# Optimization experiments

Hardware: AMD Instinct MI355X
Metric: run time of the kernel (lower is better)

## Reference

```python
import jax, jax.numpy as jnp
import numpy as np

T, D, N, W = 8192, 768, 10000, 32  # tokens, hidden dim, num spans, max span width


def setup_inputs() -> dict:
    key = jax.random.key(0)
    k1, k2, k3, k4, k5 = jax.random.split(key, 5)
    sentence_embeddings = jax.random.normal(k1, (T, D), dtype=jnp.float32)
    lengths = jax.random.randint(k2, (N,), 1, W + 1)           # span lengths in [1, W]
    starts = jax.random.randint(k3, (N,), 0, T - W)
    ends = starts + lengths - 1                                 # inclusive end, < T
    sentence_spans = jnp.stack([starts, ends], axis=1).astype(jnp.int32)
    Wq = (jax.random.normal(k4, (D, D), dtype=jnp.float32) / np.sqrt(D).astype(np.float32))
    bq = jax.random.normal(k5, (D,), dtype=jnp.float32) * 0.01
    return {"sentence_embeddings": sentence_embeddings,
            "sentence_spans": sentence_spans,
            "Wq": Wq, "bq": bq}


def reference(sentence_embeddings, sentence_spans, Wq, bq):
    # Padded + masked batched version of the per-span loop:
    #   span_emb = emb[s:e+1]; q = span_emb @ Wq.T + bq
    #   w = softmax(q @ span_emb.T, dim=1); out = (w @ span_emb).sum(0)
    starts = sentence_spans[:, 0]                               # [N]
    lengths = sentence_spans[:, 1] - starts + 1                 # inclusive end -> length
    offs = jnp.arange(W)
    pos = starts[:, None] + offs[None, :]                       # [N, W] token indices
    valid = offs[None, :] < lengths[:, None]                    # [N, W] in-span mask
    pos = jnp.clip(pos, 0, sentence_embeddings.shape[0] - 1)
    span_emb = sentence_embeddings[pos]                         # [N, W, D] ragged gather
    span_emb = jnp.where(valid[:, :, None], span_emb, 0.0)
    query = jnp.einsum('nwd,ed->nwe', span_emb, Wq) + bq        # [N, W, D]
    scores = jnp.einsum('nqd,nkd->nqk', query, span_emb)        # [N, W, W]
    scores = jnp.where(valid[:, None, :], scores, -jnp.inf)     # mask pad keys (softmax dim=1)
    weights = jax.nn.softmax(scores, axis=-1)
    attn = jnp.einsum('nqk,nkd->nqd', weights, span_emb)        # [N, W, D]
    attn = jnp.where(valid[:, :, None], attn, 0.0)              # drop pad query rows
    return attn.sum(axis=1)                                     # [N, D] == torch.sum(attention, dim=0) per span
```

## Files before the change

### kernel.cpp

```cpp
#include <hip/hip_runtime.h>
#include <hip/hip_bf16.h>
#include <cstddef>
#include <cstdint>

constexpr int Tt = 8192;
constexpr int Dd = 768;
constexpr int Nn = 10000;
constexpr int Ww = 32;

typedef __bf16 bf16x8 __attribute__((ext_vector_type(8)));
typedef __bf16 bf16x4 __attribute__((ext_vector_type(4)));
typedef __bf16 bf16x2 __attribute__((ext_vector_type(2)));
typedef _Float16 half8v __attribute__((ext_vector_type(8)));
typedef _Float16 half4v __attribute__((ext_vector_type(4)));
typedef float f32x4 __attribute__((ext_vector_type(4)));

#define MFMA16(a, b, c) __builtin_amdgcn_mfma_f32_16x16x32_bf16((a), (b), (c), 0, 0, 0)
#define MFMAH(a, b, c) __builtin_amdgcn_mfma_f32_16x16x32_f16((a), (b), (c), 0, 0, 0)

template <bool LO>
__global__ __launch_bounds__(256) void conv_kernel(const float* __restrict__ src,
                                                   __bf16* __restrict__ h,
                                                   __bf16* __restrict__ l, int n4) {
    const int i = blockIdx.x * 256 + threadIdx.x;
    if (i >= n4) return;
    const float4 v = reinterpret_cast<const float4*>(src)[i];
    bf16x4 oh, ol;
    oh[0] = (__bf16)v.x; oh[1] = (__bf16)v.y; oh[2] = (__bf16)v.z; oh[3] = (__bf16)v.w;
    reinterpret_cast<bf16x4*>(h)[i] = oh;
    if (LO) {
        ol[0] = (__bf16)(v.x - (float)oh[0]);
        ol[1] = (__bf16)(v.y - (float)oh[1]);
        ol[2] = (__bf16)(v.z - (float)oh[2]);
        ol[3] = (__bf16)(v.w - (float)oh[3]);
        reinterpret_cast<bf16x4*>(l)[i] = ol;
    }
}

__global__ __launch_bounds__(256) void conv3_kernel(const float* __restrict__ src,
                                                    __bf16* __restrict__ h,
                                                    __bf16* __restrict__ l,
                                                    _Float16* __restrict__ f, int n4) {
    const int i = blockIdx.x * 256 + threadIdx.x;
    if (i >= n4) return;
    const float4 v = reinterpret_cast<const float4*>(src)[i];
    bf16x4 oh, ol;
    half4v of;
    const float vv[4] = {v.x, v.y, v.z, v.w};
#pragma unroll
    for (int j = 0; j < 4; ++j) {
        oh[j] = (__bf16)vv[j];
        ol[j] = (__bf16)(vv[j] - (float)oh[j]);
        of[j] = (_Float16)vv[j];
    }
    reinterpret_cast<bf16x4*>(h)[i] = oh;
    reinterpret_cast<bf16x4*>(l)[i] = ol;
    reinterpret_cast<half4v*>(f)[i] = of;
}

__global__ __launch_bounds__(256) void zero_kernel(int* __restrict__ p, int n) {
    const int i = blockIdx.x * 256 + threadIdx.x;
    if (i < n) p[i] = 0;
}

__global__ __launch_bounds__(256) void hist_kernel(const int* __restrict__ spans,
                                                   int* __restrict__ hist) {
    const int i = blockIdx.x * 256 + threadIdx.x;
    if (i < Nn) atomicAdd(&hist[spans[2 * i]], 1);
}

__global__ __launch_bounds__(256) void scan_kernel(int* __restrict__ hist) {
    __shared__ int part[256];
    const int t = threadIdx.x;
    int vals[32];
    int sum = 0;
#pragma unroll
    for (int i = 0; i < 32; ++i) { vals[i] = hist[t * 32 + i]; sum += vals[i]; }
    part[t] = sum;
    __syncthreads();
    for (int off = 1; off < 256; off <<= 1) {
        const int v = (t >= off) ? part[t - off] : 0;
        __syncthreads();
        part[t] += v;
        __syncthreads();
    }
    int run = (t == 0) ? 0 : part[t - 1];
#pragma unroll
    for (int i = 0; i < 32; ++i) { const int v = vals[i]; hist[t * 32 + i] = run; run += v; }
}

__global__ __launch_bounds__(256) void scatter_kernel(const int* __restrict__ spans,
                                                      int* __restrict__ offs,
                                                      int* __restrict__ perm) {
    const int i = blockIdx.x * 256 + threadIdx.x;
    if (i < Nn) {
        const int p = atomicAdd(&offs[spans[2 * i]], 1);
        perm[p] = i;
    }
}

template <bool SPLIT>
__global__ __launch_bounds__(256) void qproj_kernel(const float* __restrict__ emb,
                                                    const float* __restrict__ Wq,
                                                    const float* __restrict__ bq,
                                                    __bf16* __restrict__ Qh,
                                                    __bf16* __restrict__ Ql) {
    __shared__ float As[64][32];
    __shared__ float Bs[64][32];
    const int tid = threadIdx.x;
    const int tx = tid & 15;
    const int ty = tid >> 4;
    const int m0 = blockIdx.x * 64;
    const int n0 = blockIdx.y * 64;

    float acc[4][4] = {};

    for (int kc = 0; kc < Dd; kc += 32) {
#pragma unroll
        for (int i = 0; i < 2; ++i) {
            const int f   = tid + i * 256;
            const int row = f >> 3;
            const int c4  = f & 7;
            const int ph  = (c4 + (row >> 2)) & 7;
            *reinterpret_cast<float4*>(&As[row][ph * 4]) =
                *reinterpret_cast<const float4*>(&emb[(size_t)(m0 + row) * Dd + kc + c4 * 4]);
            *reinterpret_cast<float4*>(&Bs[row][ph * 4]) =
                *reinterpret_cast<const float4*>(&Wq[(size_t)(n0 + row) * Dd + kc + c4 * 4]);
        }
        __syncthreads();
#pragma unroll
        for (int d4 = 0; d4 < 8; ++d4) {
            float4 av[4], bv[4];
#pragma unroll
            for (int r = 0; r < 4; ++r)
                av[r] = *reinterpret_cast<const float4*>(&As[ty * 4 + r][((d4 + ty) & 7) * 4]);
#pragma unroll
            for (int c = 0; c < 4; ++c)
                bv[c] = *reinterpret_cast<const float4*>(&Bs[tx * 4 + c][((d4 + tx) & 7) * 4]);
#pragma unroll
            for (int r = 0; r < 4; ++r)
#pragma unroll
                for (int c = 0; c < 4; ++c) {
                    acc[r][c] += av[r].x * bv[c].x;
                    acc[r][c] += av[r].y * bv[c].y;
                    acc[r][c] += av[r].z * bv[c].z;
                    acc[r][c] += av[r].w * bv[c].w;
                }
        }
        __syncthreads();
    }
#pragma unroll
    for (int r = 0; r < 4; ++r) {
        bf16x4 oh, ol;
#pragma unroll
        for (int c = 0; c < 4; ++c) {
            const float v = acc[r][c] + bq[n0 + tx * 4 + c];
            const __bf16 h = (__bf16)v;
            oh[c] = h;
            if (SPLIT) ol[c] = (__bf16)(v - (float)h);
        }
        const size_t off = (size_t)(m0 + ty * 4 + r) * Dd + n0 + tx * 4;
        *reinterpret_cast<bf16x4*>(&Qh[off]) = oh;
        if (SPLIT) *reinterpret_cast<bf16x4*>(&Ql[off]) = ol;
    }
}

__global__ __launch_bounds__(256) void qproj_mfma2_kernel(const __bf16* __restrict__ Eh,
                                                          const __bf16* __restrict__ El,
                                                          const __bf16* __restrict__ Wh,
                                                          const __bf16* __restrict__ Wl,
                                                          const float* __restrict__ bq,
                                                          _Float16* __restrict__ Qf) {
    __shared__ __align__(16) __bf16 Ahs[128 * 32];
    __shared__ __align__(16) __bf16 Als[128 * 32];
    __shared__ __align__(16) __bf16 Bhs[64 * 32];
    __shared__ __align__(16) __bf16 Bls[64 * 32];

    const int tid  = threadIdx.x;
    const int wave = tid >> 6;
    const int lane = tid & 63;

    const int b   = blockIdx.x;
    const int xcd = b & 7;
    const int li  = b >> 3;
    const int mt  = xcd * 8 + li / 12;
    const int nt  = li % 12;
    const int m0 = mt * 128;
    const int n0 = nt * 64;
    const int wm = (wave & 1) * 64;
    const int wn = (wave >> 1) * 32;
    const int fr = lane & 15;
    const int kg = lane >> 4;

    int arow[2], agc[2];
#pragma unroll
    for (int i = 0; i < 2; ++i) {
        const int seg = tid + i * 256;
        arow[i] = seg >> 2;
        agc[i]  = ((seg & 3) ^ (arow[i] & 3)) * 8;
    }
    const int brow = tid >> 2;
    const int bgc  = ((tid & 3) ^ (brow & 3)) * 8;

    bf16x8 pah[2], pal[2], pbh, pbl;
    auto ldnext = [&](int kc) {
#pragma unroll
        for (int i = 0; i < 2; ++i) {
            const size_t ga = (size_t)(m0 + arow[i]) * Dd + kc + agc[i];
            pah[i] = *reinterpret_cast<const bf16x8*>(&Eh[ga]);
            pal[i] = *reinterpret_cast<const bf16x8*>(&El[ga]);
        }
        const size_t gb = (size_t)(n0 + brow) * Dd + kc + bgc;
        pbh = *reinterpret_cast<const bf16x8*>(&Wh[gb]);
        pbl = *reinterpret_cast<const bf16x8*>(&Wl[gb]);
    };
    ldnext(0);

    f32x4 acc[4][2] = {};

    for (int kc = 0; kc < Dd; kc += 32) {
        __syncthreads();
#pragma unroll
        for (int i = 0; i < 2; ++i) {
            const int slot = tid + i * 256;
            *reinterpret_cast<bf16x8*>(&Ahs[slot * 8]) = pah[i];
            *reinterpret_cast<bf16x8*>(&Als[slot * 8]) = pal[i];
        }
        *reinterpret_cast<bf16x8*>(&Bhs[tid * 8]) = pbh;
        *reinterpret_cast<bf16x8*>(&Bls[tid * 8]) = pbl;
        __syncthreads();
        if (kc + 32 < Dd) ldnext(kc + 32);

        bf16x8 ah[4], al[4], bh[2], bl[2];
#pragma unroll
        for (int r = 0; r < 4; ++r) {
            const int R = wm + r * 16 + fr;
            const int p = (kg ^ (R & 3)) * 8;
            ah[r] = *reinterpret_cast<const bf16x8*>(&Ahs[R * 32 + p]);
            al[r] = *reinterpret_cast<const bf16x8*>(&Als[R * 32 + p]);
        }
#pragma unroll
        for (int c = 0; c < 2; ++c) {
            const int R = wn + c * 16 + fr;
            const int p = (kg ^ (R & 3)) * 8;
            bh[c] = *reinterpret_cast<const bf16x8*>(&Bhs[R * 32 + p]);
            bl[c] = *reinterpret_cast<const bf16x8*>(&Bls[R * 32 + p]);
        }
#pragma unroll
        for (int r = 0; r < 4; ++r)
#pragma unroll
            for (int c = 0; c < 2; ++c) {
                acc[r][c] = MFMA16(ah[r], bh[c], acc[r][c]);
                acc[r][c] = MFMA16(al[r], bh[c], acc[r][c]);
                acc[r][c] = MFMA16(ah[r], bl[c], acc[r][c]);
            }
    }

#pragma unroll
    for (int c = 0; c < 2; ++c) {
        const int ocol = n0 + wn + c * 16 + fr;
        const float bqv = bq[ocol];
#pragma unroll
        for (int r = 0; r < 4; ++r)
#pragma unroll
            for (int j = 0; j < 4; ++j) {
                const int orow = m0 + wm + r * 16 + kg * 4 + j;
                Qf[(size_t)orow * Dd + ocol] = (_Float16)(acc[r][c][j] + bqv);
            }
    }
}

__global__ __launch_bounds__(256) void span_attn_win_kernel(const _Float16* __restrict__ Ef,
                                                            const int* __restrict__ spans,
                                                            const _Float16* __restrict__ Qf,
                                                            const int* __restrict__ perm,
                                                            float* __restrict__ out) {
    constexpr int WR = 48, CH = 128, ST = 136, NCH = Dd / CH;
    __shared__ __align__(16) _Float16 Qs[WR * ST];
    __shared__ __align__(16) _Float16 Es[WR * ST];

    const int tid  = threadIdx.x;
    const int wave = tid >> 6;
    const int lane = tid & 63;

    const int b     = blockIdx.x;
    const int bp    = (b & 7) * 313 + (b >> 3);
    const int slot0 = bp * 4;
    const int slot  = slot0 + wave;
    const bool active = slot < Nn;

    int s0 = perm[slot0 < Nn ? slot0 : (Nn - 1)];
    if ((unsigned)s0 >= (unsigned)Nn) s0 = 0;
    int s = active ? perm[slot] : s0;
    if ((unsigned)s >= (unsigned)Nn) s = 0;

    const int w0    = spans[2 * s0];
    const int start = spans[2 * s];
    const int L     = spans[2 * s + 1] - start + 1;
    const bool big  = L > 16;
    const int sl    = start - w0;
    const bool inwin = active && sl >= 0 && sl <= (WR - 32);

    const int row = lane & 15;
    const int kq  = lane >> 4;

    const size_t gq = (size_t)(start + row) * Dd + kq * 8;

    f32x4 acc00 = {0.f, 0.f, 0.f, 0.f};
    f32x4 acc01 = {0.f, 0.f, 0.f, 0.f};
    f32x4 acc10 = {0.f, 0.f, 0.f, 0.f};
    f32x4 acc11 = {0.f, 0.f, 0.f, 0.f};

    for (int c = 0; c < NCH; ++c) {
        const int c0 = c * CH;
        __syncthreads();
#pragma unroll
        for (int i = 0; i < 3; ++i) {
            const int seg = tid + i * 256;
            const int r  = seg >> 4;
            const int cs = seg & 15;
            const int gr = w0 + r < Tt ? w0 + r : Tt - 1;
            const size_t ga = (size_t)gr * Dd + c0 + cs * 8;
            *reinterpret_cast<half8v*>(&Qs[r * ST + cs * 8]) =
                *reinterpret_cast<const half8v*>(&Qf[ga]);
            *reinterpret_cast<half8v*>(&Es[r * ST + cs * 8]) =
                *reinterpret_cast<const half8v*>(&Ef[ga]);
        }
        __syncthreads();

        if (inwin) {
            const int ab = (sl + row) * ST + kq * 8;
#pragma unroll
            for (int j = 0; j < 4; ++j) {
                const int o = j * 32;
                const half8v a0 = *reinterpret_cast<const half8v*>(&Qs[ab + o]);
                const half8v b0 = *reinterpret_cast<const half8v*>(&Es[ab + o]);
                acc00 = MFMAH(a0, b0, acc00);
                if (big) {
                    const half8v a1 = *reinterpret_cast<const half8v*>(&Qs[ab + 16 * ST + o]);
                    const half8v b1 = *reinterpret_cast<const half8v*>(&Es[ab + 16 * ST + o]);
                    acc01 = MFMAH(a0, b1, acc01);
                    acc10 = MFMAH(a1, b0, acc10);
                    acc11 = MFMAH(a1, b1, acc11);
                }
            }
        } else if (active) {
#pragma unroll
            for (int j = 0; j < 4; ++j) {
                const int o = c0 + j * 32;
                const half8v a0 = *reinterpret_cast<const half8v*>(&Qf[gq + o]);
                const half8v b0 = *reinterpret_cast<const half8v*>(&Ef[gq + o]);
                acc00 = MFMAH(a0, b0, acc00);
                if (big) {
                    const half8v a1 = *reinterpret_cast<const half8v*>(&Qf[gq + 16 * Dd + o]);
                    const half8v b1 = *reinterpret_cast<const half8v*>(&Ef[gq + 16 * Dd + o]);
                    acc01 = MFMAH(a0, b1, acc01);
                    acc10 = MFMAH(a1, b0, acc10);
                    acc11 = MFMAH(a1, b1, acc11);
                }
            }
        }
    }

    const float NEG = -1e30f;
    const bool kv0 = row < L;
    const bool kv1 = (16 + row) < L;
    float cA, cB;
    {
        float w00[4], w01[4], w10[4], w11[4];
#pragma unroll
        for (int r = 0; r < 4; ++r) {
            float m = kv0 ? acc00[r] : NEG;
            if (big) m = fmaxf(m, kv1 ? acc01[r] : NEG);
#pragma unroll
            for (int st = 1; st <= 8; st <<= 1) m = fmaxf(m, __shfl_xor(m, st));
            const float e0 = kv0 ? __expf(acc00[r] - m) : 0.f;
            const float e1 = (big && kv1) ? __expf(acc01[r] - m) : 0.f;
            float sum = e0 + e1;
#pragma unroll
            for (int st = 1; st <= 8; st <<= 1) sum += __shfl_xor(sum, st);
            const float inv = 1.f / sum;
            const bool qv = (kq * 4 + r) < L;
            w00[r] = qv ? e0 * inv : 0.f;
            w01[r] = qv ? e1 * inv : 0.f;
            if (big) {
                float mh = kv0 ? acc10[r] : NEG;
                mh = fmaxf(mh, kv1 ? acc11[r] : NEG);
#pragma unroll
                for (int st = 1; st <= 8; st <<= 1) mh = fmaxf(mh, __shfl_xor(mh, st));
                const float f0 = kv0 ? __expf(acc10[r] - mh) : 0.f;
                const float f1 = kv1 ? __expf(acc11[r] - mh) : 0.f;
                float sh = f0 + f1;
#pragma unroll
                for (int st = 1; st <= 8; st <<= 1) sh += __shfl_xor(sh, st);
                const float invh = 1.f / sh;
                const bool qvh = (16 + kq * 4 + r) < L;
                w10[r] = qvh ? f0 * invh : 0.f;
                w11[r] = qvh ? f1 * invh : 0.f;
            }
        }
        float pa = w00[0] + w00[1] + w00[2] + w00[3];
        float pb = 0.f;
        if (big) {
            pa += w10[0] + w10[1] + w10[2] + w10[3];
            pb = w01[0] + w01[1] + w01[2] + w01[3] +
                 w11[0] + w11[1] + w11[2] + w11[3];
        }
        pa += __shfl_xor(pa, 16);
        pa += __shfl_xor(pa, 32);
        if (big) {
            pb += __shfl_xor(pb, 16);
            pb += __shfl_xor(pb, 32);
        }
        cA = pa;
        cB = pb;
    }

    if (active) {
        f32x4 o[3] = {};
        const int KP = (L + 3) & ~3;
        const _Float16* ebase = Ef + (size_t)start * Dd + lane * 4;
        for (int k = 0; k < KP; k += 4) {
            float cv[4];
            half4v ev[4][3];
#pragma unroll
            for (int j = 0; j < 4; ++j) {
                const int kk = k + j;
                cv[j] = (kk < 16) ? __shfl(cA, kk) : __shfl(cB, kk - 16);
#pragma unroll
                for (int i = 0; i < 3; ++i)
                    ev[j][i] = *reinterpret_cast<const half4v*>(ebase + (size_t)kk * Dd + i * 256);
            }
#pragma unroll
            for (int j = 0; j < 4; ++j)
#pragma unroll
                for (int i = 0; i < 3; ++i) {
                    o[i][0] += cv[j] * (float)ev[j][i][0];
                    o[i][1] += cv[j] * (float)ev[j][i][1];
                    o[i][2] += cv[j] * (float)ev[j][i][2];
                    o[i][3] += cv[j] * (float)ev[j][i][3];
                }
        }
#pragma unroll
        for (int i = 0; i < 3; ++i)
            *reinterpret_cast<f32x4*>(&out[(size_t)s * Dd + i * 256 + lane * 4]) = o[i];
    }
}

template <bool SPLIT, bool SORTED>
__global__ __launch_bounds__(256) void span_attn_g_kernel(const __bf16* __restrict__ Eb,
                                                          const int* __restrict__ spans,
                                                          const __bf16* __restrict__ Qh,
                                                          const __bf16* __restrict__ Ql,
                                                          const int* __restrict__ perm,
                                                          float* __restrict__ out) {
    const int wave = threadIdx.x >> 6;
    const int lane = threadIdx.x & 63;

    int s;
    bool active;
    if (SORTED) {
        const int b    = blockIdx.x;
        const int bp   = (b & 7) * 313 + (b >> 3);
        const int slot = bp * 4 + wave;
        active = slot < Nn;
        int sv = active ? perm[slot] : 0;
        if ((unsigned)sv >= (unsigned)Nn) sv = 0;
        s = sv;
    } else {
        s = blockIdx.x * 4 + wave;
        active = true;
    }

    const int start = spans[2 * s];
    const int L     = spans[2 * s + 1] - start + 1;
    const bool big  = L > 16;

    const int row = lane & 15;
    const int kq  = lane >> 4;

    const size_t rbase = (size_t)(start + row) * Dd + kq * 8;
    const __bf16* qh0 = Qh + rbase;
    const __bf16* eb0 = Eb + rbase;
    const __bf16* ql0 = SPLIT ? (Ql + rbase) : nullptr;

    f32x4 acc00 = {0.f, 0.f, 0.f, 0.f};
    f32x4 acc01 = {0.f, 0.f, 0.f, 0.f};
    f32x4 acc10 = {0.f, 0.f, 0.f, 0.f};
    f32x4 acc11 = {0.f, 0.f, 0.f, 0.f};

    if (!big) {
        for (int kc = 0; kc < Dd; kc += 128) {
            bf16x8 A[4], B[4], AL[4];
#pragma unroll
            for (int j = 0; j < 4; ++j) {
                const int o = kc + j * 32;
                A[j] = *reinterpret_cast<const bf16x8*>(qh0 + o);
                B[j] = *reinterpret_cast<const bf16x8*>(eb0 + o);
                if (SPLIT) AL[j] = *reinterpret_cast<const bf16x8*>(ql0 + o);
            }
#pragma unroll
            for (int j = 0; j < 4; ++j) {
                acc00 = MFMA16(A[j], B[j], acc00);
                if (SPLIT) acc00 = MFMA16(AL[j], B[j], acc00);
            }
        }
    } else {
        for (int kc = 0; kc < Dd; kc += 64) {
            bf16x8 A0[2], A1[2], B0[2], B1[2], AL0[2], AL1[2];
#pragma unroll
            for (int j = 0; j < 2; ++j) {
                const int o = kc + j * 32;
                A0[j] = *reinterpret_cast<const bf16x8*>(qh0 + o);
                A1[j] = *reinterpret_cast<const bf16x8*>(qh0 + 16 * Dd + o);
                B0[j] = *reinterpret_cast<const bf16x8*>(eb0 + o);
                B1[j] = *reinterpret_cast<const bf16x8*>(eb0 + 16 * Dd + o);
                if (SPLIT) {
                    AL0[j] = *reinterpret_cast<const bf16x8*>(ql0 + o);
                    AL1[j] = *reinterpret_cast<const bf16x8*>(ql0 + 16 * Dd + o);
                }
            }
#pragma unroll
            for (int j = 0; j < 2; ++j) {
                acc00 = MFMA16(A0[j], B0[j], acc00);
                acc01 = MFMA16(A0[j], B1[j], acc01);
                acc10 = MFMA16(A1[j], B0[j], acc10);
                acc11 = MFMA16(A1[j], B1[j], acc11);
                if (SPLIT) {
                    acc00 = MFMA16(AL0[j], B0[j], acc00);
                    acc01 = MFMA16(AL0[j], B1[j], acc01);
                    acc10 = MFMA16(AL1[j], B0[j], acc10);
                    acc11 = MFMA16(AL1[j], B1[j], acc11);
                }
            }
        }
    }

    const float NEG = -1e30f;
    const bool kv0 = row < L;
    const bool kv1 = (16 + row) < L;
    float cA, cB;
    {
        float w00[4], w01[4], w10[4], w11[4];
#pragma unroll
        for (int r = 0; r < 4; ++r) {
            float m = kv0 ? acc00[r] : NEG;
            if (big) m = fmaxf(m, kv1 ? acc01[r] : NEG);
#pragma unroll
            for (int st = 1; st <= 8; st <<= 1) m = fmaxf(m, __shfl_xor(m, st));
            const float e0 = kv0 ? __expf(acc00[r] - m) : 0.f;
            const float e1 = (big && kv1) ? __expf(acc01[r] - m) : 0.f;
            float sum = e0 + e1;
#pragma unroll
            for (int st = 1; st <= 8; st <<= 1) sum += __shfl_xor(sum, st);
            const float inv = 1.f / sum;
            const bool qv = (kq * 4 + r) < L;
            w00[r] = qv ? e0 * inv : 0.f;
            w01[r] = qv ? e1 * inv : 0.f;
            if (big) {
                float mh = kv0 ? acc10[r] : NEG;
                mh = fmaxf(mh, kv1 ? acc11[r] : NEG);
#pragma unroll
                for (int st = 1; st <= 8; st <<= 1) mh = fmaxf(mh, __shfl_xor(mh, st));
                const float f0 = kv0 ? __expf(acc10[r] - mh) : 0.f;
                const float f1 = kv1 ? __expf(acc11[r] - mh) : 0.f;
                float sh = f0 + f1;
#pragma unroll
                for (int st = 1; st <= 8; st <<= 1) sh += __shfl_xor(sh, st);
                const float invh = 1.f / sh;
                const bool qvh = (16 + kq * 4 + r) < L;
                w10[r] = qvh ? f0 * invh : 0.f;
                w11[r] = qvh ? f1 * invh : 0.f;
            }
        }
        float pa = w00[0] + w00[1] + w00[2] + w00[3];
        float pb = 0.f;
        if (big) {
            pa += w10[0] + w10[1] + w10[2] + w10[3];
            pb = w01[0] + w01[1] + w01[2] + w01[3] +
                 w11[0] + w11[1] + w11[2] + w11[3];
        }
        pa += __shfl_xor(pa, 16);
        pa += __shfl_xor(pa, 32);
        if (big) {
            pb += __shfl_xor(pb, 16);
            pb += __shfl_xor(pb, 32);
        }
        cA = pa;
        cB = pb;
    }

    if (active) {
        f32x4 o[3] = {};
        const int KP = (L + 3) & ~3;
        const __bf16* ebase = Eb + (size_t)start * Dd + lane * 4;
        for (int k = 0; k < KP; k += 4) {
            float cv[4];
            bf16x4 ev[4][3];
#pragma unroll
            for (int j = 0; j < 4; ++j) {
                const int kk = k + j;
                cv[j] = (kk < 16) ? __shfl(cA, kk) : __shfl(cB, kk - 16);
#pragma unroll
                for (int i = 0; i < 3; ++i)
                    ev[j][i] = *reinterpret_cast<const bf16x4*>(ebase + (size_t)kk * Dd + i * 256);
            }
#pragma unroll
            for (int j = 0; j < 4; ++j)
#pragma unroll
                for (int i = 0; i < 3; ++i) {
                    o[i][0] += cv[j] * (float)ev[j][i][0];
                    o[i][1] += cv[j] * (float)ev[j][i][1];
                    o[i][2] += cv[j] * (float)ev[j][i][2];
                    o[i][3] += cv[j] * (float)ev[j][i][3];
                }
        }
#pragma unroll
        for (int i = 0; i < 3; ++i)
            *reinterpret_cast<f32x4*>(&out[(size_t)s * Dd + i * 256 + lane * 4]) = o[i];
    }
}

extern "C" void kernel_launch(void* const* d_in, const int* in_sizes, int n_in,
                              void* d_out, int out_size, void* d_ws, size_t ws_size,
                              hipStream_t stream) {
    const float* emb   = (const float*)d_in[0];
    const int*   spans = (const int*)d_in[1];
    const float* Wq    = (const float*)d_in[2];
    const float* bq    = (const float*)d_in[3];
    float*       out   = (float*)d_out;

    const size_t TD = (size_t)Tt * Dd;
    const size_t DD = (size_t)Dd * Dd;
    const int nInts = 8192 + 10016;
    const size_t intBytes = (size_t)nInts * sizeof(int);
    auto align16 = [](size_t x) { return (x + 15) & ~(size_t)15; };

    const size_t mainBf = align16((4 * TD + 2 * DD) * 2);
    const size_t needMain = mainBf + intBytes;
    const size_t needB = align16(3 * TD * 2) + intBytes;
    const size_t needC = 3 * TD * 2;

    if (ws_size >= needMain) {
        char* base = (char*)d_ws;
        _Float16* Qf = (_Float16*)base;
        _Float16* Ef = (_Float16*)(base + TD * 2);
        __bf16* Eh = (__bf16*)(base + 2 * TD * 2);
        __bf16* El = (__bf16*)(base + 3 * TD * 2);
        __bf16* Wh = (__bf16*)(base + 4 * TD * 2);
        __bf16* Wl = (__bf16*)(base + 4 * TD * 2 + DD * 2);
        int* hist = (int*)(base + mainBf);
        int* perm = hist + 8192;

        conv3_kernel<<<(int)(TD / 4 / 256), 256, 0, stream>>>(emb, Eh, El, Ef, (int)(TD / 4));
        conv_kernel<true><<<(int)(DD / 4 / 256), 256, 0, stream>>>(Wq, Wh, Wl, (int)(DD / 4));
        zero_kernel<<<(nInts + 255) / 256, 256, 0, stream>>>(hist, nInts);
        hist_kernel<<<40, 256, 0, stream>>>(spans, hist);
        scan_kernel<<<1, 256, 0, stream>>>(hist);
        scatter_kernel<<<40, 256, 0, stream>>>(spans, hist, perm);
        qproj_mfma2_kernel<<<768, 256, 0, stream>>>(Eh, El, Wh, Wl, bq, Qf);
        span_attn_win_kernel<<<2504, 256, 0, stream>>>(Ef, spans, Qf, perm, out);
    } else if (ws_size >= needB) {
        __bf16* w = (__bf16*)d_ws;
        __bf16* Qh = w;
        __bf16* Ql = w + TD;
        __bf16* Eh = w + 2 * TD;
        int* hist = (int*)((char*)d_ws + align16(3 * TD * 2));
        int* perm = hist + 8192;

        conv_kernel<false><<<(int)(TD / 4 / 256), 256, 0, stream>>>(emb, Eh, nullptr, (int)(TD / 4));
        zero_kernel<<<(nInts + 255) / 256, 256, 0, stream>>>(hist, nInts);
        hist_kernel<<<40, 256, 0, stream>>>(spans, hist);
        scan_kernel<<<1, 256, 0, stream>>>(hist);
        scatter_kernel<<<40, 256, 0, stream>>>(spans, hist, perm);
        qproj_kernel<true><<<dim3(Tt / 64, Dd / 64), 256, 0, stream>>>(emb, Wq, bq, Qh, Ql);
        span_attn_g_kernel<true, true><<<2504, 256, 0, stream>>>(Eh, spans, Qh, Ql, perm, out);
    } else if (ws_size >= needC) {
        __bf16* w = (__bf16*)d_ws;
        __bf16* Qh = w;
        __bf16* Ql = w + TD;
        __bf16* Eh = w + 2 * TD;
        conv_kernel<false><<<(int)(TD / 4 / 256), 256, 0, stream>>>(emb, Eh, nullptr, (int)(TD / 4));
        qproj_kernel<true><<<dim3(Tt / 64, Dd / 64), 256, 0, stream>>>(emb, Wq, bq, Qh, Ql);
        span_attn_g_kernel<true, false><<<2500, 256, 0, stream>>>(Eh, spans, Qh, Ql, nullptr, out);
    } else {
        __bf16* w = (__bf16*)d_ws;
        __bf16* Qh = w;
        __bf16* Eh = w + TD;
        conv_kernel<false><<<(int)(TD / 4 / 256), 256, 0, stream>>>(emb, Eh, nullptr, (int)(TD / 4));
        qproj_kernel<false><<<dim3(Tt / 64, Dd / 64), 256, 0, stream>>>(emb, Wq, bq, Qh, nullptr);
        span_attn_g_kernel<false, false><<<2500, 256, 0, stream>>>(Eh, spans, Qh, nullptr, nullptr, out);
    }
}
```

Before: 178.8 us.

## Fuse conversion kernels and double-buffer qproj and span attention with direct LDS loads

Merges the embedding and weight conversion kernels into one launch. The qproj kernel moves to 128x128 tiles with double-buffered shared memory filled by global_load_lds, and uses a new XOR swizzle. The span attention kernel is likewise double-buffered with direct-to-LDS loads and a swizzled, unpadded layout. The goal is to overlap global loads with MFMA work and cut launch and register-staging overhead, at the cost of more LDS per block and fewer qproj blocks in flight. The zero kernel now clears only the histogram.

```diff
diff --git a/kernel.cpp b/kernel.cpp
--- a/kernel.cpp
+++ b/kernel.cpp
@@ -10,13 +10,63 @@
 
 typedef __bf16 bf16x8 __attribute__((ext_vector_type(8)));
 typedef __bf16 bf16x4 __attribute__((ext_vector_type(4)));
-typedef __bf16 bf16x2 __attribute__((ext_vector_type(2)));
 typedef _Float16 half8v __attribute__((ext_vector_type(8)));
 typedef _Float16 half4v __attribute__((ext_vector_type(4)));
 typedef float f32x4 __attribute__((ext_vector_type(4)));
 
 #define MFMA16(a, b, c) __builtin_amdgcn_mfma_f32_16x16x32_bf16((a), (b), (c), 0, 0, 0)
 #define MFMAH(a, b, c) __builtin_amdgcn_mfma_f32_16x16x32_f16((a), (b), (c), 0, 0, 0)
+
+template <typename T>
+__device__ inline void gll16(const T* g, T* l) {
+    __builtin_amdgcn_global_load_lds(
+        (const __attribute__((address_space(1))) void*)g,
+        (__attribute__((address_space(3))) void*)l, 16, 0, 0);
+}
+__device__ inline void vmdrain() {
+    asm volatile("s_waitcnt vmcnt(0)" ::: "memory");
+}
+
+__global__ __launch_bounds__(256) void conv_fused_kernel(const float* __restrict__ emb,
+                                                         const float* __restrict__ Wq,
+                                                         __bf16* __restrict__ Eh,
+                                                         __bf16* __restrict__ El,
+                                                         _Float16* __restrict__ Ef,
+                                                         __bf16* __restrict__ Wh,
+                                                         __bf16* __restrict__ Wl) {
+    const int nE = (Tt * Dd) / 4;
+    const int nW = (Dd * Dd) / 4;
+    const int i = blockIdx.x * 256 + threadIdx.x;
+    if (i < nE) {
+        const float4 v = reinterpret_cast<const float4*>(emb)[i];
+        const float vv[4] = {v.x, v.y, v.z, v.w};
+        bf16x4 oh, ol;
+        half4v of;
+#pragma unroll
+        for (int j = 0; j < 4; ++j) {
+            oh[j] = (__bf16)vv[j];
+            ol[j] = (__bf16)(vv[j] - (float)oh[j]);
+            of[j] = (_Float16)vv[j];
+        }
+        reinterpret_cast<bf16x4*>(Eh)[i] = oh;
+        reinterpret_cast<bf16x4*>(El)[i] = ol;
+        reinterpret_cast<half4v*>(Ef)[i] = of;
+    } else {
+        const int j4 = i - nE;
+        if (j4 < nW) {
+            const float4 v = reinterpret_cast<const float4*>(Wq)[j4];
+            const float vv[4] = {v.x, v.y, v.z, v.w};
+            bf16x4 oh, ol;
+#pragma unroll
+            for (int j = 0; j < 4; ++j) {
+                oh[j] = (__bf16)vv[j];
+                ol[j] = (__bf16)(vv[j] - (float)oh[j]);
+            }
+            reinterpret_cast<bf16x4*>(Wh)[j4] = oh;
+            reinterpret_cast<bf16x4*>(Wl)[j4] = ol;
+        }
+    }
+}
 
 template <bool LO>
 __global__ __launch_bounds__(256) void conv_kernel(const float* __restrict__ src,
@@ -37,27 +87,6 @@
     }
 }
 
-__global__ __launch_bounds__(256) void conv3_kernel(const float* __restrict__ src,
-                                                    __bf16* __restrict__ h,
-                                                    __bf16* __restrict__ l,
-                                                    _Float16* __restrict__ f, int n4) {
-    const int i = blockIdx.x * 256 + threadIdx.x;
-    if (i >= n4) return;
-    const float4 v = reinterpret_cast<const float4*>(src)[i];
-    bf16x4 oh, ol;
-    half4v of;
-    const float vv[4] = {v.x, v.y, v.z, v.w};
-#pragma unroll
-    for (int j = 0; j < 4; ++j) {
-        oh[j] = (__bf16)vv[j];
-        ol[j] = (__bf16)(vv[j] - (float)oh[j]);
-        of[j] = (_Float16)vv[j];
-    }
-    reinterpret_cast<bf16x4*>(h)[i] = oh;
-    reinterpret_cast<bf16x4*>(l)[i] = ol;
-    reinterpret_cast<half4v*>(f)[i] = of;
-}
-
 __global__ __launch_bounds__(256) void zero_kernel(int* __restrict__ p, int n) {
     const int i = blockIdx.x * 256 + threadIdx.x;
     if (i < n) p[i] = 0;
@@ -165,16 +194,16 @@
     }
 }
 
-__global__ __launch_bounds__(256) void qproj_mfma2_kernel(const __bf16* __restrict__ Eh,
+__global__ __launch_bounds__(256) void qproj_mfma3_kernel(const __bf16* __restrict__ Eh,
                                                           const __bf16* __restrict__ El,
                                                           const __bf16* __restrict__ Wh,
                                                           const __bf16* __restrict__ Wl,
                                                           const float* __restrict__ bq,
                                                           _Float16* __restrict__ Qf) {
-    __shared__ __align__(16) __bf16 Ahs[128 * 32];
-    __shared__ __align__(16) __bf16 Als[128 * 32];
-    __shared__ __align__(16) __bf16 Bhs[64 * 32];
-    __shared__ __align__(16) __bf16 Bls[64 * 32];
+    __shared__ __align__(16) __bf16 Ahs[2][128 * 32];
+    __shared__ __align__(16) __bf16 Als[2][128 * 32];
+    __shared__ __align__(16) __bf16 Bhs[2][128 * 32];
+    __shared__ __align__(16) __bf16 Bls[2][128 * 32];
 
     const int tid  = threadIdx.x;
     const int wave = tid >> 6;
@@ -183,73 +212,65 @@
     const int b   = blockIdx.x;
     const int xcd = b & 7;
     const int li  = b >> 3;
-    const int mt  = xcd * 8 + li / 12;
-    const int nt  = li % 12;
+    const int mt  = xcd * 8 + li / 6;
+    const int nt  = li % 6;
     const int m0 = mt * 128;
-    const int n0 = nt * 64;
+    const int n0 = nt * 128;
     const int wm = (wave & 1) * 64;
-    const int wn = (wave >> 1) * 32;
+    const int wn = (wave >> 1) * 64;
     const int fr = lane & 15;
     const int kg = lane >> 4;
 
-    int arow[2], agc[2];
+    int srow[2], sgc[2];
 #pragma unroll
     for (int i = 0; i < 2; ++i) {
-        const int seg = tid + i * 256;
-        arow[i] = seg >> 2;
-        agc[i]  = ((seg & 3) ^ (arow[i] & 3)) * 8;
-    }
-    const int brow = tid >> 2;
-    const int bgc  = ((tid & 3) ^ (brow & 3)) * 8;
-
-    bf16x8 pah[2], pal[2], pbh, pbl;
-    auto ldnext = [&](int kc) {
+        const int s = tid + i * 256;
+        srow[i] = s >> 2;
+        sgc[i]  = ((s & 3) ^ ((srow[i] >> 1) & 3)) * 8;
+    }
+
+    auto issue = [&](int kc, int buf) {
 #pragma unroll
         for (int i = 0; i < 2; ++i) {
-            const size_t ga = (size_t)(m0 + arow[i]) * Dd + kc + agc[i];
-            pah[i] = *reinterpret_cast<const bf16x8*>(&Eh[ga]);
-            pal[i] = *reinterpret_cast<const bf16x8*>(&El[ga]);
-        }
-        const size_t gb = (size_t)(n0 + brow) * Dd + kc + bgc;
-        pbh = *reinterpret_cast<const bf16x8*>(&Wh[gb]);
-        pbl = *reinterpret_cast<const bf16x8*>(&Wl[gb]);
+            const int s = tid + i * 256;
+            const size_t ga = (size_t)(m0 + srow[i]) * Dd + kc + sgc[i];
+            const size_t gb = (size_t)(n0 + srow[i]) * Dd + kc + sgc[i];
+            gll16(Eh + ga, &Ahs[buf][s * 8]);
+            gll16(El + ga, &Als[buf][s * 8]);
+            gll16(Wh + gb, &Bhs[buf][s * 8]);
+            gll16(Wl + gb, &Bls[buf][s * 8]);
+        }
     };
-    ldnext(0);
-
-    f32x4 acc[4][2] = {};
+
+    issue(0, 0);
+
+    f32x4 acc[4][4] = {};
 
     for (int kc = 0; kc < Dd; kc += 32) {
+        const int buf = (kc >> 5) & 1;
+        vmdrain();
         __syncthreads();
-#pragma unroll
-        for (int i = 0; i < 2; ++i) {
-            const int slot = tid + i * 256;
-            *reinterpret_cast<bf16x8*>(&Ahs[slot * 8]) = pah[i];
-            *reinterpret_cast<bf16x8*>(&Als[slot * 8]) = pal[i];
-        }
-        *reinterpret_cast<bf16x8*>(&Bhs[tid * 8]) = pbh;
-        *reinterpret_cast<bf16x8*>(&Bls[tid * 8]) = pbl;
-        __syncthreads();
-        if (kc + 32 < Dd) ldnext(kc + 32);
-
-        bf16x8 ah[4], al[4], bh[2], bl[2];
+        if (kc + 32 < Dd) issue(kc + 32, buf ^ 1);
+
+        bf16x8 ah[4], al[4], bh[4], bl[4];
 #pragma unroll
         for (int r = 0; r < 4; ++r) {
             const int R = wm + r * 16 + fr;
-            const int p = (kg ^ (R & 3)) * 8;
-            ah[r] = *reinterpret_cast<const bf16x8*>(&Ahs[R * 32 + p]);
-            al[r] = *reinterpret_cast<const bf16x8*>(&Als[R * 32 + p]);
-        }
-#pragma unroll
-        for (int c = 0; c < 2; ++c) {
+            const int p = (kg ^ ((R >> 1) & 3)) * 8;
+            ah[r] = *reinterpret_cast<const bf16x8*>(&Ahs[buf][R * 32 + p]);
+            al[r] = *reinterpret_cast<const bf16x8*>(&Als[buf][R * 32 + p]);
+        }
+#pragma unroll
+        for (int c = 0; c < 4; ++c) {
             const int R = wn + c * 16 + fr;
-            const int p = (kg ^ (R & 3)) * 8;
-            bh[c] = *reinterpret_cast<const bf16x8*>(&Bhs[R * 32 + p]);
-            bl[c] = *reinterpret_cast<const bf16x8*>(&Bls[R * 32 + p]);
+            const int p = (kg ^ ((R >> 1) & 3)) * 8;
+            bh[c] = *reinterpret_cast<const bf16x8*>(&Bhs[buf][R * 32 + p]);
+            bl[c] = *reinterpret_cast<const bf16x8*>(&Bls[buf][R * 32 + p]);
         }
 #pragma unroll
         for (int r = 0; r < 4; ++r)
 #pragma unroll
-            for (int c = 0; c < 2; ++c) {
+            for (int c = 0; c < 4; ++c) {
                 acc[r][c] = MFMA16(ah[r], bh[c], acc[r][c]);
                 acc[r][c] = MFMA16(al[r], bh[c], acc[r][c]);
                 acc[r][c] = MFMA16(ah[r], bl[c], acc[r][c]);
@@ -257,7 +278,7 @@
     }
 
 #pragma unroll
-    for (int c = 0; c < 2; ++c) {
+    for (int c = 0; c < 4; ++c) {
         const int ocol = n0 + wn + c * 16 + fr;
         const float bqv = bq[ocol];
 #pragma unroll
@@ -270,14 +291,14 @@
     }
 }
 
-__global__ __launch_bounds__(256) void span_attn_win_kernel(const _Float16* __restrict__ Ef,
-                                                            const int* __restrict__ spans,
-                                                            const _Float16* __restrict__ Qf,
-                                                            const int* __restrict__ perm,
-                                                            float* __restrict__ out) {
-    constexpr int WR = 48, CH = 128, ST = 136, NCH = Dd / CH;
-    __shared__ __align__(16) _Float16 Qs[WR * ST];
-    __shared__ __align__(16) _Float16 Es[WR * ST];
+__global__ __launch_bounds__(256) void span_attn_win2_kernel(const _Float16* __restrict__ Ef,
+                                                             const int* __restrict__ spans,
+                                                             const _Float16* __restrict__ Qf,
+                                                             const int* __restrict__ perm,
+                                                             float* __restrict__ out) {
+    constexpr int WR = 48, CH = 128, NCH = Dd / CH;
+    __shared__ __align__(16) _Float16 Qs[2][WR * CH];
+    __shared__ __align__(16) _Float16 Es[2][WR * CH];
 
     const int tid  = threadIdx.x;
     const int wave = tid >> 6;
@@ -306,45 +327,59 @@
 
     const size_t gq = (size_t)(start + row) * Dd + kq * 8;
 
+    int srow[3], sgc[3];
+#pragma unroll
+    for (int i = 0; i < 3; ++i) {
+        const int sg = tid + i * 256;
+        srow[i] = sg >> 4;
+        sgc[i]  = ((sg & 15) ^ (srow[i] & 7)) * 8;
+    }
+    auto issue = [&](int c, int buf) {
+        const int c0 = c * CH;
+#pragma unroll
+        for (int i = 0; i < 3; ++i) {
+            const int sg = tid + i * 256;
+            int gr = w0 + srow[i];
+            if (gr > Tt - 1) gr = Tt - 1;
+            const size_t ga = (size_t)gr * Dd + c0 + sgc[i];
+            gll16(Qf + ga, &Qs[buf][sg * 8]);
+            gll16(Ef + ga, &Es[buf][sg * 8]);
+        }
+    };
+
+    issue(0, 0);
+
     f32x4 acc00 = {0.f, 0.f, 0.f, 0.f};
     f32x4 acc01 = {0.f, 0.f, 0.f, 0.f};
     f32x4 acc10 = {0.f, 0.f, 0.f, 0.f};
     f32x4 acc11 = {0.f, 0.f, 0.f, 0.f};
 
     for (int c = 0; c < NCH; ++c) {
-        const int c0 = c * CH;
+        const int buf = c & 1;
+        vmdrain();
         __syncthreads();
-#pragma unroll
-        for (int i = 0; i < 3; ++i) {
-            const int seg = tid + i * 256;
-            const int r  = seg >> 4;
-            const int cs = seg & 15;
-            const int gr = w0 + r < Tt ? w0 + r : Tt - 1;
-            const size_t ga = (size_t)gr * Dd + c0 + cs * 8;
-            *reinterpret_cast<half8v*>(&Qs[r * ST + cs * 8]) =
-                *reinterpret_cast<const half8v*>(&Qf[ga]);
-            *reinterpret_cast<half8v*>(&Es[r * ST + cs * 8]) =
-                *reinterpret_cast<const half8v*>(&Ef[ga]);
-        }
-        __syncthreads();
+        if (c + 1 < NCH) issue(c + 1, buf ^ 1);
 
         if (inwin) {
-            const int ab = (sl + row) * ST + kq * 8;
 #pragma unroll
             for (int j = 0; j < 4; ++j) {
-                const int o = j * 32;
-                const half8v a0 = *reinterpret_cast<const half8v*>(&Qs[ab + o]);
-                const half8v b0 = *reinterpret_cast<const half8v*>(&Es[ab + o]);
+                const int R0 = sl + row;
+                const int p0 = ((kq + 4 * j) ^ (R0 & 7)) * 8;
+                const half8v a0 = *reinterpret_cast<const half8v*>(&Qs[buf][R0 * CH + p0]);
+                const half8v b0 = *reinterpret_cast<const half8v*>(&Es[buf][R0 * CH + p0]);
                 acc00 = MFMAH(a0, b0, acc00);
                 if (big) {
-                    const half8v a1 = *reinterpret_cast<const half8v*>(&Qs[ab + 16 * ST + o]);
-                    const half8v b1 = *reinterpret_cast<const half8v*>(&Es[ab + 16 * ST + o]);
+                    const int R1 = R0 + 16;
+                    const int p1 = ((kq + 4 * j) ^ (R1 & 7)) * 8;
+                    const half8v a1 = *reinterpret_cast<const half8v*>(&Qs[buf][R1 * CH + p1]);
+                    const half8v b1 = *reinterpret_cast<const half8v*>(&Es[buf][R1 * CH + p1]);
                     acc01 = MFMAH(a0, b1, acc01);
                     acc10 = MFMAH(a1, b0, acc10);
                     acc11 = MFMAH(a1, b1, acc11);
                 }
             }
         } else if (active) {
+            const int c0 = c * CH;
 #pragma unroll
             for (int j = 0; j < 4; ++j) {
                 const int o = c0 + j * 32;
@@ -652,14 +687,14 @@
         int* hist = (int*)(base + mainBf);
         int* perm = hist + 8192;
 
-        conv3_kernel<<<(int)(TD / 4 / 256), 256, 0, stream>>>(emb, Eh, El, Ef, (int)(TD / 4));
-        conv_kernel<true><<<(int)(DD / 4 / 256), 256, 0, stream>>>(Wq, Wh, Wl, (int)(DD / 4));
-        zero_kernel<<<(nInts + 255) / 256, 256, 0, stream>>>(hist, nInts);
+        const int convBlocks = (int)((TD / 4 + DD / 4) / 256);
+        conv_fused_kernel<<<convBlocks, 256, 0, stream>>>(emb, Wq, Eh, El, Ef, Wh, Wl);
+        zero_kernel<<<32, 256, 0, stream>>>(hist, 8192);
         hist_kernel<<<40, 256, 0, stream>>>(spans, hist);
         scan_kernel<<<1, 256, 0, stream>>>(hist);
         scatter_kernel<<<40, 256, 0, stream>>>(spans, hist, perm);
-        qproj_mfma2_kernel<<<768, 256, 0, stream>>>(Eh, El, Wh, Wl, bq, Qf);
-        span_attn_win_kernel<<<2504, 256, 0, stream>>>(Ef, spans, Qf, perm, out);
+        qproj_mfma3_kernel<<<384, 256, 0, stream>>>(Eh, El, Wh, Wl, bq, Qf);
+        span_attn_win2_kernel<<<2504, 256, 0, stream>>>(Ef, spans, Qf, perm, out);
     } else if (ws_size >= needB) {
         __bf16* w = (__bf16*)d_ws;
         __bf16* Qh = w;
@@ -669,7 +704,7 @@
         int* perm = hist + 8192;
 
         conv_kernel<false><<<(int)(TD / 4 / 256), 256, 0, stream>>>(emb, Eh, nullptr, (int)(TD / 4));
-        zero_kernel<<<(nInts + 255) / 256, 256, 0, stream>>>(hist, nInts);
+        zero_kernel<<<32, 256, 0, stream>>>(hist, 8192);
         hist_kernel<<<40, 256, 0, stream>>>(spans, hist);
         scan_kernel<<<1, 256, 0, stream>>>(hist);
         scatter_kernel<<<40, 256, 0, stream>>>(spans, hist, perm);
```

After: 182.9 us. +2.3%, slower.
